# Kernel optimization log

Hardware: AMD Instinct MI355X
Metric: run time of the kernel (lower is better)

## Reference

```python
import jax, jax.numpy as jnp
import numpy as np

MAX_DEGREE = 8
N_COEFF = 45  # sum of (2l+1) over even l <= 8
N_DIRS = 100
BATCH = 16384


def _make_ls(max_degree, n_coeff):
    ls = np.zeros(n_coeff, dtype=np.int32)
    for degree in range(0, max_degree + 1, 2):
        for order in range(-degree, degree + 1):
            ls[degree * (degree + 1) // 2 + order] = degree
    return jnp.asarray(ls)


def _sconv(x, w, ls):
    # Faithful to: sqrt(pi/(2l+1)) * w[:, :, l//2] * x, summed over input channels.
    lfac = jnp.sqrt(jnp.pi / (2.0 * ls.astype(x.dtype) + 1.0))  # [C]
    we = w[:, :, ls // 2] * lfac  # [O, I, C]
    return jnp.einsum('oic,bic->boc', we, x)  # [B, O, C]


def _nonlin(x, sft, isft):
    # (sft @ relu(isft @ x[..., None])).squeeze(-1)
    y = jax.nn.relu(jnp.einsum('dc,bic->bid', isft, x))  # [B, I, D]
    return jnp.einsum('cd,bid->bic', sft, y)  # [B, I, C]


def setup_inputs() -> dict:
    key = jax.random.key(0)
    ks = jax.random.split(key, 12)

    def xav(k, shape):
        fan_in = shape[1] * shape[2]
        fan_out = shape[0] * shape[2]
        bound = float(np.sqrt(6.0 / (fan_in + fan_out)))
        return jax.random.uniform(k, shape, jnp.float32, -bound, bound)

    inp = {
        'x': jax.random.normal(ks[0], (BATCH, 4, N_COEFF), jnp.float32),
        'sft': jax.random.normal(ks[1], (N_COEFF, N_DIRS), jnp.float32) * 0.1,
        'isft': jax.random.normal(ks[2], (N_DIRS, N_COEFF), jnp.float32) * 0.1,
        'w1': xav(ks[3], (16, 4, 5)),
        'w2': xav(ks[4], (32, 16, 5)),
        'w3': xav(ks[5], (64, 32, 5)),
        'w4': xav(ks[6], (128, 64, 5)),
        'w5': xav(ks[7], (64, 128, 5)),
        'w6': xav(ks[8], (32, 128, 5)),
        'w7': xav(ks[9], (16, 64, 5)),
        'w8': xav(ks[10], (16, 32, 5)),
        'w9': xav(ks[11], (1, 16, 5)),
        'ls': _make_ls(MAX_DEGREE, N_COEFF),
    }
    return inp


def reference(x, sft, isft, w1, w2, w3, w4, w5, w6, w7, w8, w9, ls):
    e1 = _nonlin(_sconv(x, w1, ls), sft, isft)
    e2 = _nonlin(_sconv(e1, w2, ls), sft, isft)
    e3 = _nonlin(_sconv(e2, w3, ls), sft, isft)
    e4 = _nonlin(_sconv(e3, w4, ls), sft, isft)
    d1 = _nonlin(jnp.concatenate([_sconv(e4, w5, ls), e3], axis=1), sft, isft)
    d2 = _nonlin(jnp.concatenate([_sconv(d1, w6, ls), e2], axis=1), sft, isft)
    d3 = _nonlin(jnp.concatenate([_sconv(d2, w7, ls), e1], axis=1), sft, isft)
    d4 = _nonlin(_sconv(d3, w8, ls), sft, isft)
    d5 = _sconv(d4, w9, ls)  # [B, 1, C]
    return jnp.squeeze(d5)  # [B, C]
```

## Files before the change

kernel.cpp:

```cpp
#include <hip/hip_runtime.h>
#include <math.h>


typedef _Float16 half_t;
typedef _Float16 f16x8 __attribute__((ext_vector_type(8)));
typedef _Float16 f16x4 __attribute__((ext_vector_type(4)));
typedef __fp16 h2 __attribute__((ext_vector_type(2)));
typedef float f32x4 __attribute__((ext_vector_type(4)));
typedef unsigned int u32;

#define PRB 272
#define NPAIRS 120
#define E1R 128
#define E2R 144
#define E3R 176

#define WS_FRAG_U32 6656
#define WS_AFRAG_U32 64000
#define WS_NEEDED ((WS_FRAG_U32 + WS_AFRAG_U32) * 4)

__device__ __host__ __forceinline__ constexpr int l_of(int c) {
  return (c >= 1) + (c >= 6) + (c >= 15) + (c >= 28);
}
__device__ __forceinline__ float lfac_of(int l) {
  return sqrtf(3.14159265358979323846f / (float)(4 * l + 1));
}
__device__ __forceinline__ u32 pk2(float a, float b) {
  auto v = __builtin_amdgcn_cvt_pkrtz(a, b);
  return __builtin_bit_cast(u32, v);
}
__device__ __forceinline__ u32 pk2rne(float a, float b) {
  unsigned short lo = __builtin_bit_cast(unsigned short, (half_t)a);
  unsigned short hi = __builtin_bit_cast(unsigned short, (half_t)b);
  return (u32)lo | ((u32)hi << 16);
}
__device__ __forceinline__ u32 pkrelu(float a, float b) {
#if defined(__has_builtin) && __has_builtin(__builtin_elementwise_max)
  u32 v = pk2(a, b);
  h2 hv = __builtin_bit_cast(h2, v);
  h2 z = {};
  hv = __builtin_elementwise_max(hv, z);
  return __builtin_bit_cast(u32, hv);
#else
  return pk2(fmaxf(a, 0.f), fmaxf(b, 0.f));
#endif
}
__device__ __forceinline__ float dot2(u32 xp, u32 wp, float acc) {
#if __has_builtin(__builtin_amdgcn_fdot2)
  return __builtin_amdgcn_fdot2(__builtin_bit_cast(h2, xp), __builtin_bit_cast(h2, wp), acc, false);
#else
  h2 xv = __builtin_bit_cast(h2, xp), wv = __builtin_bit_cast(h2, wp);
  return acc + (float)xv[0] * (float)wv[0] + (float)xv[1] * (float)wv[1];
#endif
}
__device__ __forceinline__ u32 mergepair(u32 a, u32 b, int par) {
  return par ? ((a >> 16) | (b & 0xffff0000u))
             : ((a & 0x0000ffffu) | (b << 16));
}
__device__ __forceinline__ f32x4 mfma16(f16x8 a, f16x8 b, f32x4 c) {
  return __builtin_amdgcn_mfma_f32_16x16x32_f16(a, b, c, 0, 0, 0);
}
__device__ __forceinline__ f32x4 mfma16x16(f16x4 a, f16x4 b, f32x4 c) {
  return __builtin_amdgcn_mfma_f32_16x16x16f16(a, b, c, 0, 0, 0);
}

struct Frags {
  f16x8 a1[7][2];
};

__device__ __forceinline__ f16x8 ldpair8(const char* base, int par) {
  const uint4 q0 = *(const uint4*)(base);
  const uint4 q1 = *(const uint4*)(base + 16);
  uint4 r;
  r.x = mergepair(q0.x, q0.y, par);
  r.y = mergepair(q0.z, q0.w, par);
  r.z = mergepair(q1.x, q1.y, par);
  r.w = mergepair(q1.z, q1.w, par);
  return __builtin_bit_cast(f16x8, r);
}

template <bool TW>
__device__ void nonlin_tiles(const Frags& F, const uint4* __restrict__ p2,
                             const float* __restrict__ sft,
                             char* smem, int lane, int wid,
                             int T, int TA, int inArow, int inBrow,
                             int outArow, int outBrow) {
  const int i15 = lane & 15, g = lane >> 4;
  for (int t = wid; t < T; t += 4) {
    const int inrow = (t < TA) ? (inArow + t * 16) : (inBrow + (t - TA) * 16);
    const int outrow = (t < TA) ? (outArow + t * 16) : (outBrow + (t - TA) * 16);
    const int R = inrow + i15, par = R & 1;
    const char* ib = smem + (R >> 1) * PRB + g * 32;
    f16x8 b0 = ldpair8(ib, par);
    f16x8 b1 = ldpair8(ib + 128, par);
    f32x4 acc1[7];
#pragma unroll
    for (int mt = 0; mt < 7; ++mt) {
      f32x4 z = {0.f, 0.f, 0.f, 0.f};
      z = mfma16(F.a1[mt][0], b0, z);
      acc1[mt] = mfma16(F.a1[mt][1], b1, z);
    }
    u32 pk[7][2];
#pragma unroll
    for (int kt = 0; kt < 7; ++kt) {
      pk[kt][0] = pkrelu(acc1[kt][0], acc1[kt][1]);
      pk[kt][1] = pkrelu(acc1[kt][2], acc1[kt][3]);
    }
    f32x4 acc2[3];
#pragma unroll
    for (int n = 0; n < 3; ++n) acc2[n] = (f32x4){0.f, 0.f, 0.f, 0.f};
#pragma unroll
    for (int q = 0; q < 4; ++q) {
      uint2 yw0; yw0.x = pk[2 * q][0]; yw0.y = pk[2 * q][1];
      const f16x4 yA = __builtin_bit_cast(f16x4, yw0);
      f16x4 yB = {};
      if (q < 3) {
        uint2 yw1; yw1.x = pk[2 * q + 1][0]; yw1.y = pk[2 * q + 1][1];
        yB = __builtin_bit_cast(f16x4, yw1);
      }
#pragma unroll
      for (int n = 0; n < 3; ++n) {
        f16x4 bA, bB;
        if constexpr (TW) {
          const uint4 aw = p2[(n * 4 + q) * 64 + lane];
          uint2 lo; lo.x = aw.x; lo.y = aw.y;
          uint2 hi; hi.x = aw.z; hi.y = aw.w;
          bA = __builtin_bit_cast(f16x4, lo);
          bB = __builtin_bit_cast(f16x4, hi);
        } else {
          const int c0 = 16 * n + i15;
#pragma unroll
          for (int j = 0; j < 4; ++j) {
            const int dA = 32 * q + 4 * g + j;
            bA[j] = (half_t)((c0 < 45 && dA < 100) ? sft[c0 * 100 + dA] : 0.f);
            const int dB = 32 * q + 16 + 4 * g + j;
            bB[j] = (half_t)((c0 < 45 && dB < 100) ? sft[c0 * 100 + dB] : 0.f);
          }
        }
        acc2[n] = mfma16x16(yA, bA, acc2[n]);
        if (q < 3) acc2[n] = mfma16x16(yB, bB, acc2[n]);
      }
    }
    char* ob = smem + ((outrow >> 1) + 2 * g) * PRB + i15 * 4;
#pragma unroll
    for (int n = 0; n < 3; ++n) {
      *(u32*)(ob + n * 64) = pk2(acc2[n][0], acc2[n][1]);
      *(u32*)(ob + PRB + n * 64) = pk2(acc2[n][2], acc2[n][3]);
    }
  }
}

template <int O, int I, int SPL, bool INPLACE>
__device__ void sconv_mfma(const uint4* __restrict__ afr, char* smem,
                           int lane, int wid, int inArow, int inBrow, int outrow) {
  constexpr int Mt = O / 16;
  constexpr int Kt = (I + 31) / 32;
  constexpr int CELLS = Mt * 6;
  constexpr int NCI = (CELLS + 3) / 4;
  constexpr bool CONCAT = (SPL < I);
  const int n15 = lane & 15, g = lane >> 4;

  f32x4 accs[INPLACE ? NCI : 1];

#pragma unroll
  for (int ci = 0; ci < NCI; ++ci) {
    const int cell = wid + 4 * ci;
    if (cell < CELLS) {
      const int mt = cell / 6, grp = cell - 6 * mt;
      const int l = (grp >= 1) + (grp >= 2) + (grp >= 3) + (grp >= 4);
      const int c0 = l * (2 * l - 1) + ((grp == 5) ? 16 : 0);
      const int c = c0 + n15;
      f32x4 acc = {0.f, 0.f, 0.f, 0.f};
#pragma unroll
      for (int kt = 0; kt < Kt; ++kt) {
        const f16x8 A = __builtin_bit_cast(f16x8, afr[((l * Mt + mt) * Kt + kt) * 64 + lane]);
        int basepair;
        if constexpr (CONCAT) {
          const int iA0 = 32 * kt + 8 * g;
          basepair = ((iA0 < SPL) ? (inArow + iA0) : (inBrow + iA0 - SPL)) >> 1;
        } else {
          basepair = (inArow >> 1) + 16 * kt + 4 * g;
        }
        const char* bp = smem + basepair * PRB + c * 4;
        uint4 b4;
        b4.x = *(const u32*)(bp);
        b4.y = *(const u32*)(bp + PRB);
        b4.z = *(const u32*)(bp + 2 * PRB);
        b4.w = *(const u32*)(bp + 3 * PRB);
        acc = mfma16(A, __builtin_bit_cast(f16x8, b4), acc);
      }
      if constexpr (INPLACE) {
        accs[ci] = acc;
      } else {
        const int sz = (grp == 4) ? 16 : (((grp == 0) || (grp == 5)) ? 1 : (4 * l + 1));
        if (n15 < sz) {
          char* wb = smem + ((outrow >> 1) + 8 * mt + 2 * g) * PRB + c * 4;
          *(u32*)(wb) = pk2(acc[0], acc[1]);
          *(u32*)(wb + PRB) = pk2(acc[2], acc[3]);
        }
      }
    }
  }
  if constexpr (INPLACE) {
    __syncthreads();
#pragma unroll
    for (int ci = 0; ci < NCI; ++ci) {
      const int cell = wid + 4 * ci;
      if (cell < CELLS) {
        const int mt = cell / 6, grp = cell - 6 * mt;
        const int l = (grp >= 1) + (grp >= 2) + (grp >= 3) + (grp >= 4);
        const int c0 = l * (2 * l - 1) + ((grp == 5) ? 16 : 0);
        const int sz = (grp == 4) ? 16 : (((grp == 0) || (grp == 5)) ? 1 : (4 * l + 1));
        const int c = c0 + n15;
        if (n15 < sz) {
          char* wb = smem + ((outrow >> 1) + 8 * mt + 2 * g) * PRB + c * 4;
          *(u32*)(wb) = pk2(accs[ci][0], accs[ci][1]);
          *(u32*)(wb + PRB) = pk2(accs[ci][2], accs[ci][3]);
        }
      }
    }
  }
  __syncthreads();
}

template <int O, int I, int SPL, int NSEG, int NIP, int SEG>
__device__ __forceinline__ void sconv_acc_p(const float* __restrict__ wf, int o, int ip,
                                            bool act, const char* smem, int inArow, int inBrow,
                                            float* acc) {
  constexpr int NC = 48 / NSEG;
  constexpr int NU4 = NC / 4;
  constexpr int C0 = SEG * NC;
#pragma unroll
  for (int k = 0; k < NC; ++k) acc[k] = 0.f;
  if (!act) return;
#pragma unroll 2
  for (int p = ip; p < I / 2; p += NIP) {
    const int rA = 2 * p;
    const char* rb = smem +
        (((rA < SPL) ? ((inArow >> 1) + p) : ((inBrow >> 1) + p - SPL / 2)) * PRB) + C0 * 4;
    u32 wv[5];
#pragma unroll
    for (int l = 0; l < 5; ++l)
      wv[l] = pk2rne(wf[(o * I + rA) * 5 + l], wf[(o * I + rA + 1) * 5 + l]);
#pragma unroll
    for (int k = 0; k < NU4; ++k) {
      const uint4 q = *(const uint4*)(rb + k * 16);
      const u32 qq[4] = {q.x, q.y, q.z, q.w};
#pragma unroll
      for (int j = 0; j < 4; ++j) {
        const int c = C0 + k * 4 + j;
        acc[k * 4 + j] = dot2(qq[j], wv[l_of(c)], acc[k * 4 + j]);
      }
    }
  }
}

template <int NSEG, int SEG>
__device__ __forceinline__ void sconv_write_p(char* smem, int outrow, int o, const float* acc) {
  constexpr int NC = 48 / NSEG;
  constexpr int C0 = SEG * NC;
  const int R = outrow + o;
  char* wb = smem + (R >> 1) * PRB + (R & 1) * 2 + C0 * 4;
#pragma unroll
  for (int k = 0; k < NC; ++k) {
    const int c = C0 + k;
    *(half_t*)(wb + k * 4) = (half_t)(acc[k] * lfac_of(l_of(c)));
  }
}

template <int O, int I, int SPL, int NSEG, int NIP>
__device__ void sconv_layer(const float* __restrict__ wf, char* smem, int tid,
                            int inArow, int inBrow, int outrow) {
  constexpr int NC = 48 / NSEG;
  const int ip = (NIP == 1) ? 0 : (tid % NIP);
  const int seg = (tid / NIP) % NSEG;
  const int o = tid / (NIP * NSEG);
  const bool act = (o < O);
  float acc[NC];
  if (seg == 0)
    sconv_acc_p<O, I, SPL, NSEG, NIP, 0>(wf, o, ip, act, smem, inArow, inBrow, acc);
  else if (seg == 1)
    sconv_acc_p<O, I, SPL, NSEG, NIP, 1>(wf, o, ip, act, smem, inArow, inBrow, acc);
  else if constexpr (NSEG > 2) {
    sconv_acc_p<O, I, SPL, NSEG, NIP, 2>(wf, o, ip, act, smem, inArow, inBrow, acc);
  }
  if constexpr (NIP >= 2) {
#pragma unroll
    for (int k = 0; k < NC; ++k) acc[k] += __shfl_xor(acc[k], 1);
  }
  if constexpr (NIP >= 4) {
#pragma unroll
    for (int k = 0; k < NC; ++k) acc[k] += __shfl_xor(acc[k], 2);
  }
  __syncthreads();
  if (act && ip == 0) {
    if (seg == 0) sconv_write_p<NSEG, 0>(smem, outrow, o, acc);
    else if (seg == 1) sconv_write_p<NSEG, 1>(smem, outrow, o, acc);
    else if constexpr (NSEG > 2) { sconv_write_p<NSEG, 2>(smem, outrow, o, acc); }
  }
  __syncthreads();
}

__global__ void scnn_prep(const float* __restrict__ sft, const float* __restrict__ isft,
                          const float* __restrict__ w1, const float* __restrict__ w2,
                          const float* __restrict__ w3, const float* __restrict__ w4,
                          const float* __restrict__ w5, const float* __restrict__ w6,
                          const float* __restrict__ w7, const float* __restrict__ w8,
                          const float* __restrict__ w9, u32* __restrict__ wsbuf) {
  const int gid = blockIdx.x * 256 + threadIdx.x;
  if (gid < 3584) {
    const int f = gid >> 8, r = gid & 255, ln = r >> 2, wd = r & 3;
    const int mt = f >> 1, kt = f & 1;
    const int d = 16 * mt + (ln & 15);
    const int c = 32 * kt + 8 * (ln >> 4) + 2 * wd;
    const float v0 = (d < 100 && c < 45) ? isft[d * 45 + c] : 0.f;
    const float v1 = (d < 100 && c + 1 < 45) ? isft[d * 45 + c + 1] : 0.f;
    wsbuf[gid] = pk2rne(v0, v1);
  } else if (gid < WS_FRAG_U32) {
    const int e = gid - 3584;
    const int f = e >> 8, r = e & 255, ln = r >> 2, wd = r & 3;
    const int m = f >> 2, q = f & 3;
    const int kt = 2 * q + (wd >> 1);
    const int c = 16 * m + (ln & 15);
    const int d = 16 * kt + 4 * (ln >> 4) + 2 * (wd & 1);
    const float v0 = (kt < 7 && c < 45 && d < 100) ? sft[c * 100 + d] : 0.f;
    const float v1 = (kt < 7 && c < 45 && d + 1 < 100) ? sft[c * 100 + d + 1] : 0.f;
    wsbuf[gid] = pk2rne(v0, v1);
  } else if (gid < WS_FRAG_U32 + WS_AFRAG_U32) {
    const int e = gid - WS_FRAG_U32;
    const int frag = e >> 8, r = e & 255, ln = r >> 2, wd = r & 3;
    const float* src; int O, I, Mt, Kt, off;
    if (frag < 5)        { src = w1; O = 16;  I = 4;   Mt = 1; Kt = 1; off = 0;   }
    else if (frag < 15)  { src = w2; O = 32;  I = 16;  Mt = 2; Kt = 1; off = 5;   }
    else if (frag < 35)  { src = w3; O = 64;  I = 32;  Mt = 4; Kt = 1; off = 15;  }
    else if (frag < 115) { src = w4; O = 128; I = 64;  Mt = 8; Kt = 2; off = 35;  }
    else if (frag < 195) { src = w5; O = 64;  I = 128; Mt = 4; Kt = 4; off = 115; }
    else if (frag < 235) { src = w6; O = 32;  I = 128; Mt = 2; Kt = 4; off = 195; }
    else if (frag < 245) { src = w7; O = 16;  I = 64;  Mt = 1; Kt = 2; off = 235; }
    else                 { src = w8; O = 16;  I = 32;  Mt = 1; Kt = 1; off = 245; }
    const int fl = frag - off;
    const int l = fl / (Mt * Kt), rem = fl % (Mt * Kt);
    const int mt = rem / Kt, kt = rem % Kt;
    const int o = 16 * mt + (ln & 15);
    const int i0 = 32 * kt + 8 * (ln >> 4) + 2 * wd;
    const float lf = lfac_of(l);
    const float v0 = (i0 < I) ? src[(o * I + i0) * 5 + l] * lf : 0.f;
    const float v1 = (i0 + 1 < I) ? src[(o * I + i0 + 1) * 5 + l] * lf : 0.f;
    wsbuf[gid] = pk2rne(v0, v1);
  }
  (void)w9;
}

template <bool TW>
__global__ __launch_bounds__(256, 3) void scnn_mfma(
    const float* __restrict__ x, const float* __restrict__ sft, const float* __restrict__ isft,
    const float* __restrict__ w1, const float* __restrict__ w2, const float* __restrict__ w3,
    const float* __restrict__ w4, const float* __restrict__ w5, const float* __restrict__ w6,
    const float* __restrict__ w7, const float* __restrict__ w8, const float* __restrict__ w9,
    const u32* __restrict__ wsbuf, float* __restrict__ out) {
  __shared__ __align__(16) char smem[NPAIRS * PRB];
  const int tid = threadIdx.x, lane = tid & 63, wid = tid >> 6, b = blockIdx.x;
  const uint4* p2 = TW ? ((const uint4*)wsbuf) + 14 * 64 : nullptr;
  const uint4* afrB = TW ? ((const uint4*)wsbuf) + (WS_FRAG_U32 / 4) : nullptr;

  Frags F;
  if constexpr (TW) {
    const uint4* p1 = (const uint4*)wsbuf;
#pragma unroll
    for (int f = 0; f < 14; ++f)
      F.a1[f / 2][f % 2] = __builtin_bit_cast(f16x8, p1[f * 64 + lane]);
  } else {
    const int i15 = lane & 15, g = lane >> 4;
#pragma unroll
    for (int mt = 0; mt < 7; ++mt)
#pragma unroll
      for (int kt = 0; kt < 2; ++kt) {
        const int d = 16 * mt + i15;
        f16x8 v;
#pragma unroll
        for (int j = 0; j < 8; ++j) {
          const int c = 32 * kt + 8 * g + j;
          v[j] = (half_t)((d < 100 && c < 45) ? isft[d * 45 + c] : 0.f);
        }
        F.a1[mt][kt] = v;
      }
  }

  for (int idx = tid; idx < (NPAIRS * PRB) / 4; idx += 256)
    ((u32*)smem)[idx] = 0u;
  __syncthreads();
  if (tid < 192) {
    const int r = tid / 48, c = tid % 48;
    const float v = (c < 45) ? x[b * 180 + r * 45 + c] : 0.f;
    *(half_t*)(smem + (r >> 1) * PRB + c * 4 + (r & 1) * 2) = (half_t)v;
  }
  __syncthreads();

  if constexpr (TW) {
    sconv_mfma<16, 4, 4, true>(afrB + 0 * 64, smem, lane, wid, 0, 0, 0);
    nonlin_tiles<TW>(F, p2, sft, smem, lane, wid, 1, 1, 0, 0, E1R, E1R);
    __syncthreads();
    sconv_mfma<32, 16, 16, false>(afrB + 5 * 64, smem, lane, wid, E1R, E1R, 0);
    nonlin_tiles<TW>(F, p2, sft, smem, lane, wid, 2, 2, 0, 0, E2R, E2R);
    __syncthreads();
    sconv_mfma<64, 32, 32, false>(afrB + 15 * 64, smem, lane, wid, E2R, E2R, 0);
    nonlin_tiles<TW>(F, p2, sft, smem, lane, wid, 4, 4, 0, 0, E3R, E3R);
    __syncthreads();
    sconv_mfma<128, 64, 64, false>(afrB + 35 * 64, smem, lane, wid, E3R, E3R, 0);
    nonlin_tiles<TW>(F, p2, sft, smem, lane, wid, 8, 8, 0, 0, 0, 0);
    __syncthreads();
    sconv_mfma<64, 128, 128, true>(afrB + 115 * 64, smem, lane, wid, 0, 0, 0);
    nonlin_tiles<TW>(F, p2, sft, smem, lane, wid, 8, 4, 0, E3R, 0, E3R);
    __syncthreads();
    sconv_mfma<32, 128, 64, true>(afrB + 195 * 64, smem, lane, wid, 0, E3R, 0);
    nonlin_tiles<TW>(F, p2, sft, smem, lane, wid, 4, 2, 0, E2R, 0, E2R);
    __syncthreads();
    sconv_mfma<16, 64, 32, true>(afrB + 235 * 64, smem, lane, wid, 0, E2R, 0);
    nonlin_tiles<TW>(F, p2, sft, smem, lane, wid, 2, 1, 0, E1R, 0, E1R);
    __syncthreads();
    sconv_mfma<16, 32, 16, true>(afrB + 245 * 64, smem, lane, wid, 0, E1R, 0);
    nonlin_tiles<TW>(F, p2, sft, smem, lane, wid, 1, 1, 0, 0, 0, 0);
    __syncthreads();
  } else {
    sconv_layer<16, 4, 4, 3, 4>(w1, smem, tid, 0, 0, 0);
    nonlin_tiles<TW>(F, p2, sft, smem, lane, wid, 1, 1, 0, 0, E1R, E1R);
    __syncthreads();
    sconv_layer<32, 16, 16, 2, 4>(w2, smem, tid, E1R, E1R, 0);
    nonlin_tiles<TW>(F, p2, sft, smem, lane, wid, 2, 2, 0, 0, E2R, E2R);
    __syncthreads();
    sconv_layer<64, 32, 32, 2, 2>(w3, smem, tid, E2R, E2R, 0);
    nonlin_tiles<TW>(F, p2, sft, smem, lane, wid, 4, 4, 0, 0, E3R, E3R);
    __syncthreads();
    sconv_layer<128, 64, 64, 2, 1>(w4, smem, tid, E3R, E3R, 0);
    nonlin_tiles<TW>(F, p2, sft, smem, lane, wid, 8, 8, 0, 0, 0, 0);
    __syncthreads();
    sconv_layer<64, 128, 128, 2, 2>(w5, smem, tid, 0, 0, 0);
    nonlin_tiles<TW>(F, p2, sft, smem, lane, wid, 8, 4, 0, E3R, 0, E3R);
    __syncthreads();
    sconv_layer<32, 128, 64, 2, 4>(w6, smem, tid, 0, E3R, 0);
    nonlin_tiles<TW>(F, p2, sft, smem, lane, wid, 4, 2, 0, E2R, 0, E2R);
    __syncthreads();
    sconv_layer<16, 64, 32, 3, 4>(w7, smem, tid, 0, E2R, 0);
    nonlin_tiles<TW>(F, p2, sft, smem, lane, wid, 2, 1, 0, E1R, 0, E1R);
    __syncthreads();
    sconv_layer<16, 32, 16, 3, 4>(w8, smem, tid, 0, E1R, 0);
    nonlin_tiles<TW>(F, p2, sft, smem, lane, wid, 1, 1, 0, 0, 0, 0);
    __syncthreads();
  }

  if (tid < 45) {
    const int c = tid, l = l_of(c);
    float acc = 0.f;
#pragma unroll
    for (int i = 0; i < 16; ++i)
      acc += w9[i * 5 + l] *
             (float)(*(const half_t*)(smem + (i >> 1) * PRB + c * 4 + (i & 1) * 2));
    out[b * 45 + c] = acc * lfac_of(l);
  }
}

extern "C" void kernel_launch(void* const* d_in, const int* in_sizes, int n_in,
                              void* d_out, int out_size, void* d_ws, size_t ws_size,
                              hipStream_t stream) {
  (void)n_in; (void)out_size;
  const float* x    = (const float*)d_in[0];
  const float* sft  = (const float*)d_in[1];
  const float* isft = (const float*)d_in[2];
  const float* w1 = (const float*)d_in[3];
  const float* w2 = (const float*)d_in[4];
  const float* w3 = (const float*)d_in[5];
  const float* w4 = (const float*)d_in[6];
  const float* w5 = (const float*)d_in[7];
  const float* w6 = (const float*)d_in[8];
  const float* w7 = (const float*)d_in[9];
  const float* w8 = (const float*)d_in[10];
  const float* w9 = (const float*)d_in[11];
  float* out = (float*)d_out;

  const int batch = in_sizes[0] / 180;

  if (ws_size >= (size_t)WS_NEEDED) {
    u32* wsbuf = (u32*)d_ws;
    const int prepN = WS_FRAG_U32 + WS_AFRAG_U32;
    hipLaunchKernelGGL(scnn_prep, dim3((prepN + 255) / 256), dim3(256), 0, stream,
                       sft, isft, w1, w2, w3, w4, w5, w6, w7, w8, w9, wsbuf);
    hipLaunchKernelGGL((scnn_mfma<true>), dim3(batch), dim3(256), 0, stream,
                       x, sft, isft, w1, w2, w3, w4, w5, w6, w7, w8, w9, wsbuf, out);
  } else {
    hipLaunchKernelGGL((scnn_mfma<false>), dim3(batch), dim3(256), 0, stream,
                       x, sft, isft, w1, w2, w3, w4, w5, w6, w7, w8, w9,
                       (const u32*)nullptr, out);
  }
}
```

Baseline: 584.0 us.

## Process two batch elements per 512-thread block with doubled shared activation buffers

Replaces the one-sample-per-block 256-thread MFMA kernel with a 512-thread kernel in which each block handles two batch samples, each with its own shared-memory activation region. Work cells and nonlinearity tiles from both samples are spread across 8 waves, which gives each wave more independent MFMA work per barrier and halves the number of barrier phases per sample. The cost is twice the LDS per block, which can limit how many blocks fit on a CU. A dead duplicate kernel (scnn_mfma2) with no output write is also added, and an odd batch size falls back to the scalar path.

```diff
diff --git a/kernel.cpp b/kernel.cpp
--- a/kernel.cpp
+++ b/kernel.cpp
@@ -11,6 +11,7 @@
 
 #define PRB 272
 #define NPAIRS 120
+#define ACTB (NPAIRS * PRB)
 #define E1R 128
 #define E2R 144
 #define E3R 176
@@ -77,6 +78,261 @@
   r.z = mergepair(q1.x, q1.y, par);
   r.w = mergepair(q1.z, q1.w, par);
   return __builtin_bit_cast(f16x8, r);
+}
+
+__device__ void nonlin_tiles2(const Frags& F, const uint4* __restrict__ p2,
+                              char* smem, int lane, int wid,
+                              int T, int TA, int inArow, int inBrow,
+                              int outArow, int outBrow) {
+  const int i15 = lane & 15, g = lane >> 4;
+  for (int t = wid; t < 2 * T; t += 8) {
+    const int e = (t >= T) ? 1 : 0;
+    const int tt = t - (e ? T : 0);
+    char* sm = smem + e * ACTB;
+    const int inrow = (tt < TA) ? (inArow + tt * 16) : (inBrow + (tt - TA) * 16);
+    const int outrow = (tt < TA) ? (outArow + tt * 16) : (outBrow + (tt - TA) * 16);
+    const int R = inrow + i15, par = R & 1;
+    const char* ib = sm + (R >> 1) * PRB + g * 32;
+    f16x8 b0 = ldpair8(ib, par);
+    f16x8 b1 = ldpair8(ib + 128, par);
+    f32x4 acc1[7];
+#pragma unroll
+    for (int mt = 0; mt < 7; ++mt) {
+      f32x4 z = {0.f, 0.f, 0.f, 0.f};
+      z = mfma16(F.a1[mt][0], b0, z);
+      acc1[mt] = mfma16(F.a1[mt][1], b1, z);
+    }
+    u32 pk[7][2];
+#pragma unroll
+    for (int kt = 0; kt < 7; ++kt) {
+      pk[kt][0] = pkrelu(acc1[kt][0], acc1[kt][1]);
+      pk[kt][1] = pkrelu(acc1[kt][2], acc1[kt][3]);
+    }
+    f32x4 acc2[3];
+#pragma unroll
+    for (int n = 0; n < 3; ++n) acc2[n] = (f32x4){0.f, 0.f, 0.f, 0.f};
+#pragma unroll
+    for (int q = 0; q < 4; ++q) {
+      uint2 yw0; yw0.x = pk[2 * q][0]; yw0.y = pk[2 * q][1];
+      const f16x4 yA = __builtin_bit_cast(f16x4, yw0);
+      f16x4 yB = {};
+      if (q < 3) {
+        uint2 yw1; yw1.x = pk[2 * q + 1][0]; yw1.y = pk[2 * q + 1][1];
+        yB = __builtin_bit_cast(f16x4, yw1);
+      }
+#pragma unroll
+      for (int n = 0; n < 3; ++n) {
+        const uint4 aw = p2[(n * 4 + q) * 64 + lane];
+        uint2 lo; lo.x = aw.x; lo.y = aw.y;
+        uint2 hi; hi.x = aw.z; hi.y = aw.w;
+        const f16x4 bA = __builtin_bit_cast(f16x4, lo);
+        const f16x4 bB = __builtin_bit_cast(f16x4, hi);
+        acc2[n] = mfma16x16(yA, bA, acc2[n]);
+        if (q < 3) acc2[n] = mfma16x16(yB, bB, acc2[n]);
+      }
+    }
+    char* ob = sm + ((outrow >> 1) + 2 * g) * PRB + i15 * 4;
+#pragma unroll
+    for (int n = 0; n < 3; ++n) {
+      *(u32*)(ob + n * 64) = pk2(acc2[n][0], acc2[n][1]);
+      *(u32*)(ob + PRB + n * 64) = pk2(acc2[n][2], acc2[n][3]);
+    }
+  }
+}
+
+template <int O, int I, int SPL, bool INPLACE>
+__device__ void sconv_mfma2(const uint4* __restrict__ afr, char* smem,
+                            int lane, int wid, int inArow, int inBrow, int outrow) {
+  constexpr int Mt = O / 16;
+  constexpr int Kt = (I + 31) / 32;
+  constexpr int CELLS = Mt * 6;
+  constexpr int NCI = (2 * CELLS + 7) / 8;
+  constexpr bool CONCAT = (SPL < I);
+  const int n15 = lane & 15, g = lane >> 4;
+
+  f32x4 accs[INPLACE ? NCI : 1];
+
+#pragma unroll
+  for (int ci = 0; ci < NCI; ++ci) {
+    const int cell = wid + 8 * ci;
+    if (cell < 2 * CELLS) {
+      const int e = (cell >= CELLS) ? 1 : 0;
+      const int cl = cell - (e ? CELLS : 0);
+      char* sm = smem + e * ACTB;
+      const int mt = cl / 6, grp = cl - 6 * mt;
+      const int l = (grp >= 1) + (grp >= 2) + (grp >= 3) + (grp >= 4);
+      const int c0 = l * (2 * l - 1) + ((grp == 5) ? 16 : 0);
+      const int c = c0 + n15;
+      f32x4 acc = {0.f, 0.f, 0.f, 0.f};
+#pragma unroll
+      for (int kt = 0; kt < Kt; ++kt) {
+        const f16x8 A = __builtin_bit_cast(f16x8, afr[((l * Mt + mt) * Kt + kt) * 64 + lane]);
+        int basepair;
+        if constexpr (CONCAT) {
+          const int iA0 = 32 * kt + 8 * g;
+          basepair = ((iA0 < SPL) ? (inArow + iA0) : (inBrow + iA0 - SPL)) >> 1;
+        } else {
+          basepair = (inArow >> 1) + 16 * kt + 4 * g;
+        }
+        const char* bp = sm + basepair * PRB + c * 4;
+        uint4 b4;
+        b4.x = *(const u32*)(bp);
+        b4.y = *(const u32*)(bp + PRB);
+        b4.z = *(const u32*)(bp + 2 * PRB);
+        b4.w = *(const u32*)(bp + 3 * PRB);
+        acc = mfma16(A, __builtin_bit_cast(f16x8, b4), acc);
+      }
+      if constexpr (INPLACE) {
+        accs[ci] = acc;
+      } else {
+        const int sz = (grp == 4) ? 16 : (((grp == 0) || (grp == 5)) ? 1 : (4 * l + 1));
+        if (n15 < sz) {
+          char* wb = sm + ((outrow >> 1) + 8 * mt + 2 * g) * PRB + c * 4;
+          *(u32*)(wb) = pk2(acc[0], acc[1]);
+          *(u32*)(wb + PRB) = pk2(acc[2], acc[3]);
+        }
+      }
+    }
+  }
+  if constexpr (INPLACE) {
+    __syncthreads();
+#pragma unroll
+    for (int ci = 0; ci < NCI; ++ci) {
+      const int cell = wid + 8 * ci;
+      if (cell < 2 * CELLS) {
+        const int e = (cell >= CELLS) ? 1 : 0;
+        const int cl = cell - (e ? CELLS : 0);
+        char* sm = smem + e * ACTB;
+        const int mt = cl / 6, grp = cl - 6 * mt;
+        const int l = (grp >= 1) + (grp >= 2) + (grp >= 3) + (grp >= 4);
+        const int c0 = l * (2 * l - 1) + ((grp == 5) ? 16 : 0);
+        const int sz = (grp == 4) ? 16 : (((grp == 0) || (grp == 5)) ? 1 : (4 * l + 1));
+        const int c = c0 + n15;
+        if (n15 < sz) {
+          char* wb = sm + ((outrow >> 1) + 8 * mt + 2 * g) * PRB + c * 4;
+          *(u32*)(wb) = pk2(accs[ci][0], accs[ci][1]);
+          *(u32*)(wb + PRB) = pk2(accs[ci][2], accs[ci][3]);
+        }
+      }
+    }
+  }
+  __syncthreads();
+}
+
+__global__ __launch_bounds__(512, 2) void scnn_mfma2(
+    const float* __restrict__ x, const u32* __restrict__ wsbuf, float* __restrict__ out) {
+  __shared__ __align__(16) char smem[2 * ACTB];
+  const int tid = threadIdx.x, lane = tid & 63, wid = tid >> 6, b = blockIdx.x;
+  const uint4* p1 = (const uint4*)wsbuf;
+  const uint4* p2 = p1 + 14 * 64;
+  const uint4* afrB = ((const uint4*)wsbuf) + (WS_FRAG_U32 / 4);
+
+  Frags F;
+#pragma unroll
+  for (int f = 0; f < 14; ++f)
+    F.a1[f / 2][f % 2] = __builtin_bit_cast(f16x8, p1[f * 64 + lane]);
+
+  for (int idx = tid; idx < (2 * ACTB) / 4; idx += 512)
+    ((u32*)smem)[idx] = 0u;
+  __syncthreads();
+  if (tid < 384) {
+    const int e = tid / 192, r = (tid % 192) / 48, c = tid % 48;
+    const float v = (c < 45) ? x[(2 * b + e) * 180 + r * 45 + c] : 0.f;
+    *(half_t*)(smem + e * ACTB + (r >> 1) * PRB + c * 4 + (r & 1) * 2) = (half_t)v;
+  }
+  __syncthreads();
+
+  sconv_mfma2<16, 4, 4, true>(afrB + 0 * 64, smem, lane, wid, 0, 0, 0);
+  nonlin_tiles2(F, p2, smem, lane, wid, 1, 1, 0, 0, E1R, E1R);
+  __syncthreads();
+  sconv_mfma2<32, 16, 16, false>(afrB + 5 * 64, smem, lane, wid, E1R, E1R, 0);
+  nonlin_tiles2(F, p2, smem, lane, wid, 2, 2, 0, 0, E2R, E2R);
+  __syncthreads();
+  sconv_mfma2<64, 32, 32, false>(afrB + 15 * 64, smem, lane, wid, E2R, E2R, 0);
+  nonlin_tiles2(F, p2, smem, lane, wid, 4, 4, 0, 0, E3R, E3R);
+  __syncthreads();
+  sconv_mfma2<128, 64, 64, false>(afrB + 35 * 64, smem, lane, wid, E3R, E3R, 0);
+  nonlin_tiles2(F, p2, smem, lane, wid, 8, 8, 0, 0, 0, 0);
+  __syncthreads();
+  sconv_mfma2<64, 128, 128, true>(afrB + 115 * 64, smem, lane, wid, 0, 0, 0);
+  nonlin_tiles2(F, p2, smem, lane, wid, 8, 4, 0, E3R, 0, E3R);
+  __syncthreads();
+  sconv_mfma2<32, 128, 64, true>(afrB + 195 * 64, smem, lane, wid, 0, E3R, 0);
+  nonlin_tiles2(F, p2, smem, lane, wid, 4, 2, 0, E2R, 0, E2R);
+  __syncthreads();
+  sconv_mfma2<16, 64, 32, true>(afrB + 235 * 64, smem, lane, wid, 0, E2R, 0);
+  nonlin_tiles2(F, p2, smem, lane, wid, 2, 1, 0, E1R, 0, E1R);
+  __syncthreads();
+  sconv_mfma2<16, 32, 16, true>(afrB + 245 * 64, smem, lane, wid, 0, E1R, 0);
+  nonlin_tiles2(F, p2, smem, lane, wid, 1, 1, 0, 0, 0, 0);
+  __syncthreads();
+
+  if (tid < 90) {
+    const int e = tid / 45, c = tid % 45, l = l_of(c);
+    const char* sm = smem + e * ACTB;
+    (void)sm; (void)l;
+  }
+}
+
+__global__ __launch_bounds__(512, 2) void scnn_mfma2w(
+    const float* __restrict__ x, const float* __restrict__ w9,
+    const u32* __restrict__ wsbuf, float* __restrict__ out) {
+  __shared__ __align__(16) char smem[2 * ACTB];
+  const int tid = threadIdx.x, lane = tid & 63, wid = tid >> 6, b = blockIdx.x;
+  const uint4* p1 = (const uint4*)wsbuf;
+  const uint4* p2 = p1 + 14 * 64;
+  const uint4* afrB = ((const uint4*)wsbuf) + (WS_FRAG_U32 / 4);
+
+  Frags F;
+#pragma unroll
+  for (int f = 0; f < 14; ++f)
+    F.a1[f / 2][f % 2] = __builtin_bit_cast(f16x8, p1[f * 64 + lane]);
+
+  for (int idx = tid; idx < (2 * ACTB) / 4; idx += 512)
+    ((u32*)smem)[idx] = 0u;
+  __syncthreads();
+  if (tid < 384) {
+    const int e = tid / 192, r = (tid % 192) / 48, c = tid % 48;
+    const float v = (c < 45) ? x[(2 * b + e) * 180 + r * 45 + c] : 0.f;
+    *(half_t*)(smem + e * ACTB + (r >> 1) * PRB + c * 4 + (r & 1) * 2) = (half_t)v;
+  }
+  __syncthreads();
+
+  sconv_mfma2<16, 4, 4, true>(afrB + 0 * 64, smem, lane, wid, 0, 0, 0);
+  nonlin_tiles2(F, p2, smem, lane, wid, 1, 1, 0, 0, E1R, E1R);
+  __syncthreads();
+  sconv_mfma2<32, 16, 16, false>(afrB + 5 * 64, smem, lane, wid, E1R, E1R, 0);
+  nonlin_tiles2(F, p2, smem, lane, wid, 2, 2, 0, 0, E2R, E2R);
+  __syncthreads();
+  sconv_mfma2<64, 32, 32, false>(afrB + 15 * 64, smem, lane, wid, E2R, E2R, 0);
+  nonlin_tiles2(F, p2, smem, lane, wid, 4, 4, 0, 0, E3R, E3R);
+  __syncthreads();
+  sconv_mfma2<128, 64, 64, false>(afrB + 35 * 64, smem, lane, wid, E3R, E3R, 0);
+  nonlin_tiles2(F, p2, smem, lane, wid, 8, 8, 0, 0, 0, 0);
+  __syncthreads();
+  sconv_mfma2<64, 128, 128, true>(afrB + 115 * 64, smem, lane, wid, 0, 0, 0);
+  nonlin_tiles2(F, p2, smem, lane, wid, 8, 4, 0, E3R, 0, E3R);
+  __syncthreads();
+  sconv_mfma2<32, 128, 64, true>(afrB + 195 * 64, smem, lane, wid, 0, E3R, 0);
+  nonlin_tiles2(F, p2, smem, lane, wid, 4, 2, 0, E2R, 0, E2R);
+  __syncthreads();
+  sconv_mfma2<16, 64, 32, true>(afrB + 235 * 64, smem, lane, wid, 0, E2R, 0);
+  nonlin_tiles2(F, p2, smem, lane, wid, 2, 1, 0, E1R, 0, E1R);
+  __syncthreads();
+  sconv_mfma2<16, 32, 16, true>(afrB + 245 * 64, smem, lane, wid, 0, E1R, 0);
+  nonlin_tiles2(F, p2, smem, lane, wid, 1, 1, 0, 0, 0, 0);
+  __syncthreads();
+
+  if (tid < 90) {
+    const int e = tid / 45, c = tid % 45, l = l_of(c);
+    const char* sm = smem + e * ACTB;
+    float acc = 0.f;
+#pragma unroll
+    for (int i = 0; i < 16; ++i)
+      acc += w9[i * 5 + l] *
+             (float)(*(const half_t*)(sm + (i >> 1) * PRB + c * 4 + (i & 1) * 2));
+    out[(2 * b + e) * 45 + c] = acc * lfac_of(l);
+  }
 }
 
 template <bool TW>
@@ -150,79 +406,6 @@
   }
 }
 
-template <int O, int I, int SPL, bool INPLACE>
-__device__ void sconv_mfma(const uint4* __restrict__ afr, char* smem,
-                           int lane, int wid, int inArow, int inBrow, int outrow) {
-  constexpr int Mt = O / 16;
-  constexpr int Kt = (I + 31) / 32;
-  constexpr int CELLS = Mt * 6;
-  constexpr int NCI = (CELLS + 3) / 4;
-  constexpr bool CONCAT = (SPL < I);
-  const int n15 = lane & 15, g = lane >> 4;
-
-  f32x4 accs[INPLACE ? NCI : 1];
-
-#pragma unroll
-  for (int ci = 0; ci < NCI; ++ci) {
-    const int cell = wid + 4 * ci;
-    if (cell < CELLS) {
-      const int mt = cell / 6, grp = cell - 6 * mt;
-      const int l = (grp >= 1) + (grp >= 2) + (grp >= 3) + (grp >= 4);
-      const int c0 = l * (2 * l - 1) + ((grp == 5) ? 16 : 0);
-      const int c = c0 + n15;
-      f32x4 acc = {0.f, 0.f, 0.f, 0.f};
-#pragma unroll
-      for (int kt = 0; kt < Kt; ++kt) {
-        const f16x8 A = __builtin_bit_cast(f16x8, afr[((l * Mt + mt) * Kt + kt) * 64 + lane]);
-        int basepair;
-        if constexpr (CONCAT) {
-          const int iA0 = 32 * kt + 8 * g;
-          basepair = ((iA0 < SPL) ? (inArow + iA0) : (inBrow + iA0 - SPL)) >> 1;
-        } else {
-          basepair = (inArow >> 1) + 16 * kt + 4 * g;
-        }
-        const char* bp = smem + basepair * PRB + c * 4;
-        uint4 b4;
-        b4.x = *(const u32*)(bp);
-        b4.y = *(const u32*)(bp + PRB);
-        b4.z = *(const u32*)(bp + 2 * PRB);
-        b4.w = *(const u32*)(bp + 3 * PRB);
-        acc = mfma16(A, __builtin_bit_cast(f16x8, b4), acc);
-      }
-      if constexpr (INPLACE) {
-        accs[ci] = acc;
-      } else {
-        const int sz = (grp == 4) ? 16 : (((grp == 0) || (grp == 5)) ? 1 : (4 * l + 1));
-        if (n15 < sz) {
-          char* wb = smem + ((outrow >> 1) + 8 * mt + 2 * g) * PRB + c * 4;
-          *(u32*)(wb) = pk2(acc[0], acc[1]);
-          *(u32*)(wb + PRB) = pk2(acc[2], acc[3]);
-        }
-      }
-    }
-  }
-  if constexpr (INPLACE) {
-    __syncthreads();
-#pragma unroll
-    for (int ci = 0; ci < NCI; ++ci) {
-      const int cell = wid + 4 * ci;
-      if (cell < CELLS) {
-        const int mt = cell / 6, grp = cell - 6 * mt;
-        const int l = (grp >= 1) + (grp >= 2) + (grp >= 3) + (grp >= 4);
-        const int c0 = l * (2 * l - 1) + ((grp == 5) ? 16 : 0);
-        const int sz = (grp == 4) ? 16 : (((grp == 0) || (grp == 5)) ? 1 : (4 * l + 1));
-        const int c = c0 + n15;
-        if (n15 < sz) {
-          char* wb = smem + ((outrow >> 1) + 8 * mt + 2 * g) * PRB + c * 4;
-          *(u32*)(wb) = pk2(accs[ci][0], accs[ci][1]);
-          *(u32*)(wb + PRB) = pk2(accs[ci][2], accs[ci][3]);
-        }
-      }
-    }
-  }
-  __syncthreads();
-}
-
 template <int O, int I, int SPL, int NSEG, int NIP, int SEG>
 __device__ __forceinline__ void sconv_acc_p(const float* __restrict__ wf, int o, int ip,
                                             bool act, const char* smem, int inArow, int inBrow,
@@ -299,6 +482,78 @@
     else if constexpr (NSEG > 2) { sconv_write_p<NSEG, 2>(smem, outrow, o, acc); }
   }
   __syncthreads();
+}
+
+__global__ __launch_bounds__(256, 3) void scnn_fb(
+    const float* __restrict__ x, const float* __restrict__ sft, const float* __restrict__ isft,
+    const float* __restrict__ w1, const float* __restrict__ w2, const float* __restrict__ w3,
+    const float* __restrict__ w4, const float* __restrict__ w5, const float* __restrict__ w6,
+    const float* __restrict__ w7, const float* __restrict__ w8, const float* __restrict__ w9,
+    float* __restrict__ out) {
+  __shared__ __align__(16) char smem[NPAIRS * PRB];
+  const int tid = threadIdx.x, lane = tid & 63, wid = tid >> 6, b = blockIdx.x;
+
+  Frags F;
+  {
+    const int i15 = lane & 15, g = lane >> 4;
+#pragma unroll
+    for (int mt = 0; mt < 7; ++mt)
+#pragma unroll
+      for (int kt = 0; kt < 2; ++kt) {
+        const int d = 16 * mt + i15;
+        f16x8 v;
+#pragma unroll
+        for (int j = 0; j < 8; ++j) {
+          const int c = 32 * kt + 8 * g + j;
+          v[j] = (half_t)((d < 100 && c < 45) ? isft[d * 45 + c] : 0.f);
+        }
+        F.a1[mt][kt] = v;
+      }
+  }
+  for (int idx = tid; idx < (NPAIRS * PRB) / 4; idx += 256)
+    ((u32*)smem)[idx] = 0u;
+  __syncthreads();
+  if (tid < 192) {
+    const int r = tid / 48, c = tid % 48;
+    const float v = (c < 45) ? x[b * 180 + r * 45 + c] : 0.f;
+    *(half_t*)(smem + (r >> 1) * PRB + c * 4 + (r & 1) * 2) = (half_t)v;
+  }
+  __syncthreads();
+
+  sconv_layer<16, 4, 4, 3, 4>(w1, smem, tid, 0, 0, 0);
+  nonlin_tiles<false>(F, nullptr, sft, smem, lane, wid, 1, 1, 0, 0, E1R, E1R);
+  __syncthreads();
+  sconv_layer<32, 16, 16, 2, 4>(w2, smem, tid, E1R, E1R, 0);
+  nonlin_tiles<false>(F, nullptr, sft, smem, lane, wid, 2, 2, 0, 0, E2R, E2R);
+  __syncthreads();
+  sconv_layer<64, 32, 32, 2, 2>(w3, smem, tid, E2R, E2R, 0);
+  nonlin_tiles<false>(F, nullptr, sft, smem, lane, wid, 4, 4, 0, 0, E3R, E3R);
+  __syncthreads();
+  sconv_layer<128, 64, 64, 2, 1>(w4, smem, tid, E3R, E3R, 0);
+  nonlin_tiles<false>(F, nullptr, sft, smem, lane, wid, 8, 8, 0, 0, 0, 0);
+  __syncthreads();
+  sconv_layer<64, 128, 128, 2, 2>(w5, smem, tid, 0, 0, 0);
+  nonlin_tiles<false>(F, nullptr, sft, smem, lane, wid, 8, 4, 0, E3R, 0, E3R);
+  __syncthreads();
+  sconv_layer<32, 128, 64, 2, 4>(w6, smem, tid, 0, E3R, 0);
+  nonlin_tiles<false>(F, nullptr, sft, smem, lane, wid, 4, 2, 0, E2R, 0, E2R);
+  __syncthreads();
+  sconv_layer<16, 64, 32, 3, 4>(w7, smem, tid, 0, E2R, 0);
+  nonlin_tiles<false>(F, nullptr, sft, smem, lane, wid, 2, 1, 0, E1R, 0, E1R);
+  __syncthreads();
+  sconv_layer<16, 32, 16, 3, 4>(w8, smem, tid, 0, E1R, 0);
+  nonlin_tiles<false>(F, nullptr, sft, smem, lane, wid, 1, 1, 0, 0, 0, 0);
+  __syncthreads();
+
+  if (tid < 45) {
+    const int c = tid, l = l_of(c);
+    float acc = 0.f;
+#pragma unroll
+    for (int i = 0; i < 16; ++i)
+      acc += w9[i * 5 + l] *
+             (float)(*(const half_t*)(smem + (i >> 1) * PRB + c * 4 + (i & 1) * 2));
+    out[b * 45 + c] = acc * lfac_of(l);
+  }
 }
 
 __global__ void scnn_prep(const float* __restrict__ sft, const float* __restrict__ isft,
@@ -351,114 +606,6 @@
   (void)w9;
 }
 
-template <bool TW>
-__global__ __launch_bounds__(256, 3) void scnn_mfma(
-    const float* __restrict__ x, const float* __restrict__ sft, const float* __restrict__ isft,
-    const float* __restrict__ w1, const float* __restrict__ w2, const float* __restrict__ w3,
-    const float* __restrict__ w4, const float* __restrict__ w5, const float* __restrict__ w6,
-    const float* __restrict__ w7, const float* __restrict__ w8, const float* __restrict__ w9,
-    const u32* __restrict__ wsbuf, float* __restrict__ out) {
-  __shared__ __align__(16) char smem[NPAIRS * PRB];
-  const int tid = threadIdx.x, lane = tid & 63, wid = tid >> 6, b = blockIdx.x;
-  const uint4* p2 = TW ? ((const uint4*)wsbuf) + 14 * 64 : nullptr;
-  const uint4* afrB = TW ? ((const uint4*)wsbuf) + (WS_FRAG_U32 / 4) : nullptr;
-
-  Frags F;
-  if constexpr (TW) {
-    const uint4* p1 = (const uint4*)wsbuf;
-#pragma unroll
-    for (int f = 0; f < 14; ++f)
-      F.a1[f / 2][f % 2] = __builtin_bit_cast(f16x8, p1[f * 64 + lane]);
-  } else {
-    const int i15 = lane & 15, g = lane >> 4;
-#pragma unroll
-    for (int mt = 0; mt < 7; ++mt)
-#pragma unroll
-      for (int kt = 0; kt < 2; ++kt) {
-        const int d = 16 * mt + i15;
-        f16x8 v;
-#pragma unroll
-        for (int j = 0; j < 8; ++j) {
-          const int c = 32 * kt + 8 * g + j;
-          v[j] = (half_t)((d < 100 && c < 45) ? isft[d * 45 + c] : 0.f);
-        }
-        F.a1[mt][kt] = v;
-      }
-  }
-
-  for (int idx = tid; idx < (NPAIRS * PRB) / 4; idx += 256)
-    ((u32*)smem)[idx] = 0u;
-  __syncthreads();
-  if (tid < 192) {
-    const int r = tid / 48, c = tid % 48;
-    const float v = (c < 45) ? x[b * 180 + r * 45 + c] : 0.f;
-    *(half_t*)(smem + (r >> 1) * PRB + c * 4 + (r & 1) * 2) = (half_t)v;
-  }
-  __syncthreads();
-
-  if constexpr (TW) {
-    sconv_mfma<16, 4, 4, true>(afrB + 0 * 64, smem, lane, wid, 0, 0, 0);
-    nonlin_tiles<TW>(F, p2, sft, smem, lane, wid, 1, 1, 0, 0, E1R, E1R);
-    __syncthreads();
-    sconv_mfma<32, 16, 16, false>(afrB + 5 * 64, smem, lane, wid, E1R, E1R, 0);
-    nonlin_tiles<TW>(F, p2, sft, smem, lane, wid, 2, 2, 0, 0, E2R, E2R);
-    __syncthreads();
-    sconv_mfma<64, 32, 32, false>(afrB + 15 * 64, smem, lane, wid, E2R, E2R, 0);
-    nonlin_tiles<TW>(F, p2, sft, smem, lane, wid, 4, 4, 0, 0, E3R, E3R);
-    __syncthreads();
-    sconv_mfma<128, 64, 64, false>(afrB + 35 * 64, smem, lane, wid, E3R, E3R, 0);
-    nonlin_tiles<TW>(F, p2, sft, smem, lane, wid, 8, 8, 0, 0, 0, 0);
-    __syncthreads();
-    sconv_mfma<64, 128, 128, true>(afrB + 115 * 64, smem, lane, wid, 0, 0, 0);
-    nonlin_tiles<TW>(F, p2, sft, smem, lane, wid, 8, 4, 0, E3R, 0, E3R);
-    __syncthreads();
-    sconv_mfma<32, 128, 64, true>(afrB + 195 * 64, smem, lane, wid, 0, E3R, 0);
-    nonlin_tiles<TW>(F, p2, sft, smem, lane, wid, 4, 2, 0, E2R, 0, E2R);
-    __syncthreads();
-    sconv_mfma<16, 64, 32, true>(afrB + 235 * 64, smem, lane, wid, 0, E2R, 0);
-    nonlin_tiles<TW>(F, p2, sft, smem, lane, wid, 2, 1, 0, E1R, 0, E1R);
-    __syncthreads();
-    sconv_mfma<16, 32, 16, true>(afrB + 245 * 64, smem, lane, wid, 0, E1R, 0);
-    nonlin_tiles<TW>(F, p2, sft, smem, lane, wid, 1, 1, 0, 0, 0, 0);
-    __syncthreads();
-  } else {
-    sconv_layer<16, 4, 4, 3, 4>(w1, smem, tid, 0, 0, 0);
-    nonlin_tiles<TW>(F, p2, sft, smem, lane, wid, 1, 1, 0, 0, E1R, E1R);
-    __syncthreads();
-    sconv_layer<32, 16, 16, 2, 4>(w2, smem, tid, E1R, E1R, 0);
-    nonlin_tiles<TW>(F, p2, sft, smem, lane, wid, 2, 2, 0, 0, E2R, E2R);
-    __syncthreads();
-    sconv_layer<64, 32, 32, 2, 2>(w3, smem, tid, E2R, E2R, 0);
-    nonlin_tiles<TW>(F, p2, sft, smem, lane, wid, 4, 4, 0, 0, E3R, E3R);
-    __syncthreads();
-    sconv_layer<128, 64, 64, 2, 1>(w4, smem, tid, E3R, E3R, 0);
-    nonlin_tiles<TW>(F, p2, sft, smem, lane, wid, 8, 8, 0, 0, 0, 0);
-    __syncthreads();
-    sconv_layer<64, 128, 128, 2, 2>(w5, smem, tid, 0, 0, 0);
-    nonlin_tiles<TW>(F, p2, sft, smem, lane, wid, 8, 4, 0, E3R, 0, E3R);
-    __syncthreads();
-    sconv_layer<32, 128, 64, 2, 4>(w6, smem, tid, 0, E3R, 0);
-    nonlin_tiles<TW>(F, p2, sft, smem, lane, wid, 4, 2, 0, E2R, 0, E2R);
-    __syncthreads();
-    sconv_layer<16, 64, 32, 3, 4>(w7, smem, tid, 0, E2R, 0);
-    nonlin_tiles<TW>(F, p2, sft, smem, lane, wid, 2, 1, 0, E1R, 0, E1R);
-    __syncthreads();
-    sconv_layer<16, 32, 16, 3, 4>(w8, smem, tid, 0, E1R, 0);
-    nonlin_tiles<TW>(F, p2, sft, smem, lane, wid, 1, 1, 0, 0, 0, 0);
-    __syncthreads();
-  }
-
-  if (tid < 45) {
-    const int c = tid, l = l_of(c);
-    float acc = 0.f;
-#pragma unroll
-    for (int i = 0; i < 16; ++i)
-      acc += w9[i * 5 + l] *
-             (float)(*(const half_t*)(smem + (i >> 1) * PRB + c * 4 + (i & 1) * 2));
-    out[b * 45 + c] = acc * lfac_of(l);
-  }
-}
-
 extern "C" void kernel_launch(void* const* d_in, const int* in_sizes, int n_in,
                               void* d_out, int out_size, void* d_ws, size_t ws_size,
                               hipStream_t stream) {
@@ -479,16 +626,15 @@
 
   const int batch = in_sizes[0] / 180;
 
-  if (ws_size >= (size_t)WS_NEEDED) {
+  if (ws_size >= (size_t)WS_NEEDED && (batch % 2) == 0) {
     u32* wsbuf = (u32*)d_ws;
     const int prepN = WS_FRAG_U32 + WS_AFRAG_U32;
     hipLaunchKernelGGL(scnn_prep, dim3((prepN + 255) / 256), dim3(256), 0, stream,
                        sft, isft, w1, w2, w3, w4, w5, w6, w7, w8, w9, wsbuf);
-    hipLaunchKernelGGL((scnn_mfma<true>), dim3(batch), dim3(256), 0, stream,
-                       x, sft, isft, w1, w2, w3, w4, w5, w6, w7, w8, w9, wsbuf, out);
+    hipLaunchKernelGGL(scnn_mfma2w, dim3(batch / 2), dim3(512), 0, stream,
+                       x, w9, wsbuf, out);
   } else {
-    hipLaunchKernelGGL((scnn_mfma<false>), dim3(batch), dim3(256), 0, stream,
-                       x, sft, isft, w1, w2, w3, w4, w5, w6, w7, w8, w9,
-                       (const u32*)nullptr, out);
-  }
-}
+    hipLaunchKernelGGL(scnn_fb, dim3(batch), dim3(256), 0, stream,
+                       x, sft, isft, w1, w2, w3, w4, w5, w6, w7, w8, w9, out);
+  }
+}
```

New measurement: 894.6 us. +53.2%, slower.
